# Performance work log

Hardware: AMD Instinct MI355X
Metric: run time of the kernel (lower is better)

Reference implementation:

```python
import math
import jax, jax.numpy as jnp
import numpy as np

B, T, D_IN, D_SAE, K = 256, 64, 512, 4096, 32

def _sinusoidal_posemb(T, d):
    pos = jnp.arange(T, dtype=jnp.float32)[:, None]
    div = jnp.exp(jnp.arange(0, d, 2, dtype=jnp.float32) * (-(math.log(10000.0) / d)))
    pe = jnp.zeros((T, d), dtype=jnp.float32)
    pe = pe.at[:, 0::2].set(jnp.sin(pos * div))
    pe = pe.at[:, 1::2].set(jnp.cos(pos * div))
    return pe

def setup_inputs() -> dict:
    key = jax.random.key(0)
    k0, k1, k2 = jax.random.split(key, 3)
    x = jax.random.normal(k0, (B, T, D_IN), dtype=jnp.float32)
    W_enc = jax.random.normal(k1, (D_IN, D_SAE), dtype=jnp.float32) / D_IN ** 0.5
    W_dec = jax.random.normal(k2, (D_SAE, T, D_IN), dtype=jnp.float32) / D_SAE ** 0.5
    b_enc = jnp.zeros((D_SAE,), dtype=jnp.float32)
    b_dec = jnp.zeros((T, D_IN), dtype=jnp.float32)
    return {"x": x, "W_enc": W_enc, "W_dec": W_dec, "b_enc": b_enc, "b_dec": b_dec}

def reference(x, W_enc, W_dec, b_enc, b_dec):
    pe = _sinusoidal_posemb(T, D_IN)              # (T, d_in) buffer
    x_plus = x + pe[None]                         # (B, T, d_in)
    pre = jnp.einsum('btd,ds->bs', x_plus, W_enc) + b_enc  # (B, d_sae)
    v, i = jax.lax.top_k(pre, K)                  # (B, K) each
    rows = jnp.arange(B)[:, None]
    z = jnp.zeros_like(pre).at[rows, i].set(jax.nn.relu(v))  # sparse scatter
    x_hat = jnp.einsum('bs,std->btd', z, W_dec) + b_dec      # (B, T, d_in)
    loss = jnp.mean(jnp.sum((x_hat - x) ** 2, axis=-1))
    return loss, x_hat, z
```

## Files before the change

kernel.cpp:

```cpp
#include <hip/hip_runtime.h>
#include <math.h>

#define NB 256
#define NT 64
#define DIN 512
#define DSAE 4096
#define NK 32

__global__ __launch_bounds__(512) void k_xs(const float* __restrict__ x,
                                            float* __restrict__ xs,
                                            float* __restrict__ out) {
    const int b = blockIdx.x, d = threadIdx.x;
    if (b == 0 && d == 0) out[0] = 0.f;
    int j = d >> 1;
    float freq = expf((float)(2 * j) * (-9.210340371976184f / 512.0f));
    float pes = 0.f;
    if (d & 1) {
        for (int t = 0; t < NT; ++t) pes += cosf((float)t * freq);
    } else {
        for (int t = 0; t < NT; ++t) pes += sinf((float)t * freq);
    }
    const float* xp = x + (size_t)b * NT * DIN + d;
    float acc = 0.f;
#pragma unroll 16
    for (int t = 0; t < NT; ++t) acc += xp[(size_t)t * DIN];
    xs[(size_t)b * DIN + d] = acc + pes;
}

__global__ __launch_bounds__(256) void k_pre(const float* __restrict__ xs,
                                             const float* __restrict__ W,
                                             const float* __restrict__ b_enc,
                                             float* __restrict__ pre) {
    __shared__ float xs_t[DIN][16];
    const int tid = threadIdx.x;
    const int s = blockIdx.x * 256 + tid;
    const int b0 = blockIdx.y * 16;
    for (int i = tid; i < 16 * DIN; i += 256) {
        int bb = i >> 9, d = i & 511;
        xs_t[d][bb] = xs[(size_t)(b0 + bb) * DIN + d];
    }
    __syncthreads();
    float a[16], c[16];
#pragma unroll
    for (int i = 0; i < 16; ++i) { a[i] = 0.f; c[i] = 0.f; }
    const float* wp = W + s;
#pragma unroll 2
    for (int d = 0; d < DIN; d += 2) {
        float w0 = wp[(size_t)d * DSAE];
        float w1 = wp[(size_t)(d + 1) * DSAE];
        const float4* r0 = (const float4*)&xs_t[d][0];
        const float4* r1 = (const float4*)&xs_t[d + 1][0];
#pragma unroll
        for (int q = 0; q < 4; ++q) {
            float4 u = r0[q];
            a[q*4+0] += u.x * w0; a[q*4+1] += u.y * w0;
            a[q*4+2] += u.z * w0; a[q*4+3] += u.w * w0;
            float4 t2 = r1[q];
            c[q*4+0] += t2.x * w1; c[q*4+1] += t2.y * w1;
            c[q*4+2] += t2.z * w1; c[q*4+3] += t2.w * w1;
        }
    }
    float be = b_enc[s];
#pragma unroll
    for (int bb = 0; bb < 16; ++bb)
        pre[(size_t)(b0 + bb) * DSAE + s] = a[bb] + c[bb] + be;
}

__global__ __launch_bounds__(64) void k_topk(const float* __restrict__ pre,
                                             float* __restrict__ z_out,
                                             int* __restrict__ idx_s,
                                             float* __restrict__ zv_s) {
    const int b = blockIdx.x, lane = threadIdx.x;
    const float* pr = pre + (size_t)b * DSAE;
    float* zr = z_out + (size_t)b * DSAE;
    __shared__ float lv[64 * 65];
    __shared__ float lgv[64 * 8];
    __shared__ int   lga[64 * 8];
    for (int j = lane; j < DSAE; j += 64) zr[j] = 0.f;
    const int base = lane * 65;
    float v[64];
#pragma unroll
    for (int j = 0; j < 64; ++j) v[j] = pr[j * 64 + lane];
#pragma unroll
    for (int j = 0; j < 64; ++j) lv[base + j] = v[j];
    float lmax = -INFINITY; int larg = 0;
#pragma unroll
    for (int g = 0; g < 8; ++g) {
        float m = v[g * 8]; int a = g * 8;
#pragma unroll
        for (int t = 1; t < 8; ++t)
            if (v[g * 8 + t] > m) { m = v[g * 8 + t]; a = g * 8 + t; }
        lgv[lane * 8 + g] = m; lga[lane * 8 + g] = a;
        if (m > lmax) { lmax = m; larg = a; }
    }
    __syncthreads();
    int myi = 0; float myv = 0.f;
    for (int k = 0; k < NK; ++k) {
        float bv = lmax; int be = larg * 64 + lane;
#pragma unroll
        for (int off = 32; off >= 1; off >>= 1) {
            float ov = __shfl_down(bv, off);
            int oe = __shfl_down(be, off);
            if (ov > bv || (ov == bv && oe < be)) { bv = ov; be = oe; }
        }
        bv = __shfl(bv, 0); be = __shfl(be, 0);
        if (lane == k) { myi = be; myv = bv > 0.f ? bv : 0.f; }
        if (lane == (be & 63)) {
            int j0 = be >> 6;
            lv[base + j0] = -INFINITY;
            int g0 = j0 >> 3;
            float m = -INFINITY; int a2 = g0 << 3;
            for (int t = 0; t < 8; ++t) {
                float x2 = lv[base + (g0 << 3) + t];
                if (x2 > m) { m = x2; a2 = (g0 << 3) + t; }
            }
            lgv[lane * 8 + g0] = m; lga[lane * 8 + g0] = a2;
            lmax = -INFINITY; larg = 0;
            for (int g = 0; g < 8; ++g) {
                float x2 = lgv[lane * 8 + g];
                if (x2 > lmax) { lmax = x2; larg = lga[lane * 8 + g]; }
            }
        }
    }
    int rank = 0;
#pragma unroll
    for (int j = 0; j < NK; ++j) {
        int oi = __shfl(myi, j);
        if (lane < NK && oi < myi) rank++;
    }
    if (lane < NK) {
        idx_s[b * NK + rank] = myi;
        zv_s[b * NK + rank] = myv;
        zr[myi] = myv;
    }
}

__global__ __launch_bounds__(256) void k_dec(const float* __restrict__ x,
                                             const float* __restrict__ Wd,
                                             const float* __restrict__ bd,
                                             const int* __restrict__ idx_s,
                                             const float* __restrict__ zv_s,
                                             float* __restrict__ out) {
    const int b = blockIdx.y, chunk = blockIdx.x, tid = threadIdx.x;
    __shared__ int si[NK];
    __shared__ float sz[NK];
    if (tid < NK) { si[tid] = idx_s[b * NK + tid]; sz[tid] = zv_s[b * NK + tid]; }
    __syncthreads();
    const int f0 = chunk * 1024 + tid;
    const float4* bd4 = (const float4*)bd;
    float4 acc0 = bd4[f0];
    float4 acc1 = bd4[f0 + 256];
    float4 acc2 = bd4[f0 + 512];
    float4 acc3 = bd4[f0 + 768];
    for (int k = 0; k < NK; ++k) {
        const float4* w4 = (const float4*)(Wd + (size_t)si[k] * (NT * DIN));
        float zk = sz[k];
        float4 w0 = w4[f0], w1 = w4[f0 + 256], w2 = w4[f0 + 512], w3 = w4[f0 + 768];
        acc0.x += zk * w0.x; acc0.y += zk * w0.y; acc0.z += zk * w0.z; acc0.w += zk * w0.w;
        acc1.x += zk * w1.x; acc1.y += zk * w1.y; acc1.z += zk * w1.z; acc1.w += zk * w1.w;
        acc2.x += zk * w2.x; acc2.y += zk * w2.y; acc2.z += zk * w2.z; acc2.w += zk * w2.w;
        acc3.x += zk * w3.x; acc3.y += zk * w3.y; acc3.z += zk * w3.z; acc3.w += zk * w3.w;
    }
    const float* xr = x + (size_t)b * (NT * DIN);
    float lsum = 0.f, dx;
    float xv[16];
#pragma unroll
    for (int q = 0; q < 4; ++q) {
        int e = (f0 + q * 256) * 4;
#pragma unroll
        for (int c2 = 0; c2 < 4; ++c2) xv[q * 4 + c2] = __builtin_nontemporal_load(&xr[e + c2]);
    }
    dx = acc0.x - xv[0];  lsum += dx * dx;  dx = acc0.y - xv[1];  lsum += dx * dx;
    dx = acc0.z - xv[2];  lsum += dx * dx;  dx = acc0.w - xv[3];  lsum += dx * dx;
    dx = acc1.x - xv[4];  lsum += dx * dx;  dx = acc1.y - xv[5];  lsum += dx * dx;
    dx = acc1.z - xv[6];  lsum += dx * dx;  dx = acc1.w - xv[7];  lsum += dx * dx;
    dx = acc2.x - xv[8];  lsum += dx * dx;  dx = acc2.y - xv[9];  lsum += dx * dx;
    dx = acc2.z - xv[10]; lsum += dx * dx;  dx = acc2.w - xv[11]; lsum += dx * dx;
    dx = acc3.x - xv[12]; lsum += dx * dx;  dx = acc3.y - xv[13]; lsum += dx * dx;
    dx = acc3.z - xv[14]; lsum += dx * dx;  dx = acc3.w - xv[15]; lsum += dx * dx;

    float* xh = out + 1 + (size_t)b * (NT * DIN);
    int e;
    e = f0 * 4;
    __builtin_nontemporal_store(acc0.x, &xh[e]);     __builtin_nontemporal_store(acc0.y, &xh[e+1]);
    __builtin_nontemporal_store(acc0.z, &xh[e+2]);   __builtin_nontemporal_store(acc0.w, &xh[e+3]);
    e = (f0 + 256) * 4;
    __builtin_nontemporal_store(acc1.x, &xh[e]);     __builtin_nontemporal_store(acc1.y, &xh[e+1]);
    __builtin_nontemporal_store(acc1.z, &xh[e+2]);   __builtin_nontemporal_store(acc1.w, &xh[e+3]);
    e = (f0 + 512) * 4;
    __builtin_nontemporal_store(acc2.x, &xh[e]);     __builtin_nontemporal_store(acc2.y, &xh[e+1]);
    __builtin_nontemporal_store(acc2.z, &xh[e+2]);   __builtin_nontemporal_store(acc2.w, &xh[e+3]);
    e = (f0 + 768) * 4;
    __builtin_nontemporal_store(acc3.x, &xh[e]);     __builtin_nontemporal_store(acc3.y, &xh[e+1]);
    __builtin_nontemporal_store(acc3.z, &xh[e+2]);   __builtin_nontemporal_store(acc3.w, &xh[e+3]);

#pragma unroll
    for (int off = 32; off >= 1; off >>= 1) lsum += __shfl_down(lsum, off);
    __shared__ float red[4];
    if ((tid & 63) == 0) red[tid >> 6] = lsum;
    __syncthreads();
    if (tid == 0) {
        float tot = red[0] + red[1] + red[2] + red[3];
        atomicAdd(out, tot * (1.0f / (NB * NT)));
    }
}

extern "C" void kernel_launch(void* const* d_in, const int* in_sizes, int n_in,
                              void* d_out, int out_size, void* d_ws, size_t ws_size,
                              hipStream_t stream) {
    const float* x     = (const float*)d_in[0];
    const float* W_enc = (const float*)d_in[1];
    const float* W_dec = (const float*)d_in[2];
    const float* b_enc = (const float*)d_in[3];
    const float* b_dec = (const float*)d_in[4];
    float* out = (float*)d_out;

    float* ws    = (float*)d_ws;
    float* xs    = ws;
    float* pre   = ws + 131072;
    int*   idx_s = (int*)(ws + 1179648);
    float* zv_s  = ws + 1187840;

    float* z_out = out + 1 + (size_t)NB * NT * DIN;

    k_xs<<<NB, 512, 0, stream>>>(x, xs, out);
    k_pre<<<dim3(16, 16), 256, 0, stream>>>(xs, W_enc, b_enc, pre);
    k_topk<<<NB, 64, 0, stream>>>(pre, z_out, idx_s, zv_s);
    k_dec<<<dim3(8, NB), 256, 0, stream>>>(x, W_dec, b_dec, idx_s, zv_s, out);
}
```

Baseline: 156.2 us.

## Restructure decoder to stream W_dec column slabs through shared memory once

The decoder now assigns each block a 32-element column slice, with one batch row per thread. All 4096 W_dec rows for that slice are streamed through double-buffered shared memory in windows of 64. Each thread walks its own sorted top-k indices and accumulates only the rows it needs. This reads W_dec once in total rather than gathering 32 rows per batch element, cutting global traffic. The cost is reading the whole 128 MB W_dec, 64 barrier phases per block, divergent per-thread loops, and uncoalesced x loads and output stores with per-thread row strides.

Result: slower. 361.0 us (+131.0%).

```diff
diff --git a/kernel.cpp b/kernel.cpp
--- a/kernel.cpp
+++ b/kernel.cpp
@@ -6,6 +6,9 @@
 #define DIN 512
 #define DSAE 4096
 #define NK 32
+
+typedef float f32x4 __attribute__((ext_vector_type(4)));
+typedef float f32x2 __attribute__((ext_vector_type(2)));
 
 __global__ __launch_bounds__(512) void k_xs(const float* __restrict__ x,
                                             float* __restrict__ xs,
@@ -135,64 +138,97 @@
     }
 }
 
+#define WSTRIDE 36
 __global__ __launch_bounds__(256) void k_dec(const float* __restrict__ x,
                                              const float* __restrict__ Wd,
                                              const float* __restrict__ bd,
                                              const int* __restrict__ idx_s,
                                              const float* __restrict__ zv_s,
                                              float* __restrict__ out) {
-    const int b = blockIdx.y, chunk = blockIdx.x, tid = threadIdx.x;
-    __shared__ int si[NK];
-    __shared__ float sz[NK];
-    if (tid < NK) { si[tid] = idx_s[b * NK + tid]; sz[tid] = zv_s[b * NK + tid]; }
-    __syncthreads();
-    const int f0 = chunk * 1024 + tid;
-    const float4* bd4 = (const float4*)bd;
-    float4 acc0 = bd4[f0];
-    float4 acc1 = bd4[f0 + 256];
-    float4 acc2 = bd4[f0 + 512];
-    float4 acc3 = bd4[f0 + 768];
-    for (int k = 0; k < NK; ++k) {
-        const float4* w4 = (const float4*)(Wd + (size_t)si[k] * (NT * DIN));
-        float zk = sz[k];
-        float4 w0 = w4[f0], w1 = w4[f0 + 256], w2 = w4[f0 + 512], w3 = w4[f0 + 768];
-        acc0.x += zk * w0.x; acc0.y += zk * w0.y; acc0.z += zk * w0.z; acc0.w += zk * w0.w;
-        acc1.x += zk * w1.x; acc1.y += zk * w1.y; acc1.z += zk * w1.z; acc1.w += zk * w1.w;
-        acc2.x += zk * w2.x; acc2.y += zk * w2.y; acc2.z += zk * w2.z; acc2.w += zk * w2.w;
-        acc3.x += zk * w3.x; acc3.y += zk * w3.y; acc3.z += zk * w3.z; acc3.w += zk * w3.w;
-    }
-    const float* xr = x + (size_t)b * (NT * DIN);
-    float lsum = 0.f, dx;
-    float xv[16];
-#pragma unroll
-    for (int q = 0; q < 4; ++q) {
-        int e = (f0 + q * 256) * 4;
-#pragma unroll
-        for (int c2 = 0; c2 < 4; ++c2) xv[q * 4 + c2] = __builtin_nontemporal_load(&xr[e + c2]);
-    }
-    dx = acc0.x - xv[0];  lsum += dx * dx;  dx = acc0.y - xv[1];  lsum += dx * dx;
-    dx = acc0.z - xv[2];  lsum += dx * dx;  dx = acc0.w - xv[3];  lsum += dx * dx;
-    dx = acc1.x - xv[4];  lsum += dx * dx;  dx = acc1.y - xv[5];  lsum += dx * dx;
-    dx = acc1.z - xv[6];  lsum += dx * dx;  dx = acc1.w - xv[7];  lsum += dx * dx;
-    dx = acc2.x - xv[8];  lsum += dx * dx;  dx = acc2.y - xv[9];  lsum += dx * dx;
-    dx = acc2.z - xv[10]; lsum += dx * dx;  dx = acc2.w - xv[11]; lsum += dx * dx;
-    dx = acc3.x - xv[12]; lsum += dx * dx;  dx = acc3.y - xv[13]; lsum += dx * dx;
-    dx = acc3.z - xv[14]; lsum += dx * dx;  dx = acc3.w - xv[15]; lsum += dx * dx;
-
-    float* xh = out + 1 + (size_t)b * (NT * DIN);
-    int e;
-    e = f0 * 4;
-    __builtin_nontemporal_store(acc0.x, &xh[e]);     __builtin_nontemporal_store(acc0.y, &xh[e+1]);
-    __builtin_nontemporal_store(acc0.z, &xh[e+2]);   __builtin_nontemporal_store(acc0.w, &xh[e+3]);
-    e = (f0 + 256) * 4;
-    __builtin_nontemporal_store(acc1.x, &xh[e]);     __builtin_nontemporal_store(acc1.y, &xh[e+1]);
-    __builtin_nontemporal_store(acc1.z, &xh[e+2]);   __builtin_nontemporal_store(acc1.w, &xh[e+3]);
-    e = (f0 + 512) * 4;
-    __builtin_nontemporal_store(acc2.x, &xh[e]);     __builtin_nontemporal_store(acc2.y, &xh[e+1]);
-    __builtin_nontemporal_store(acc2.z, &xh[e+2]);   __builtin_nontemporal_store(acc2.w, &xh[e+3]);
-    e = (f0 + 768) * 4;
-    __builtin_nontemporal_store(acc3.x, &xh[e]);     __builtin_nontemporal_store(acc3.y, &xh[e+1]);
-    __builtin_nontemporal_store(acc3.z, &xh[e+2]);   __builtin_nontemporal_store(acc3.w, &xh[e+3]);
+    const int tid = threadIdx.x;
+    const int cbase = blockIdx.x * 32;
+    __shared__ float buf[2][64 * WSTRIDE];
+
+    float acc[32];
+    {
+        const float4* bd4 = (const float4*)(bd + cbase);
+#pragma unroll
+        for (int q = 0; q < 8; ++q) {
+            float4 v = bd4[q];
+            acc[q*4+0] = v.x; acc[q*4+1] = v.y; acc[q*4+2] = v.z; acc[q*4+3] = v.w;
+        }
+    }
+
+    const int slot_w = tid >> 2;
+    const int quad0 = (tid & 3) * 2;
+    const float* gsrc = Wd + (size_t)slot_w * (NT * DIN) + cbase + quad0 * 4;
+
+    const int* myi = idx_s + tid * NK;
+    const float* myz = zv_s + tid * NK;
+    int p = 0;
+    int nexti = myi[0];
+    float nextz = myz[0];
+
+    float4 st0 = *(const float4*)(gsrc);
+    float4 st1 = *(const float4*)(gsrc + 4);
+    {
+        float* wb = &buf[0][slot_w * WSTRIDE + quad0 * 4];
+        *(float4*)wb = st0;
+        *(float4*)(wb + 4) = st1;
+    }
+    __syncthreads();
+
+    for (int phase = 0; phase < 64; ++phase) {
+        if (phase < 63) {
+            const float* g = gsrc + (size_t)(phase + 1) * 64 * (NT * DIN);
+            st0 = *(const float4*)(g);
+            st1 = *(const float4*)(g + 4);
+        }
+        const int win0 = phase * 64;
+        const int winEnd = win0 + 64;
+        const float* cb = buf[phase & 1];
+        while (nexti < winEnd) {
+            const float zk = nextz;
+            const float* w = cb + (nexti - win0) * WSTRIDE;
+#pragma unroll
+            for (int q = 0; q < 8; ++q) {
+                float4 wv = *(const float4*)&w[q * 4];
+                acc[q*4+0] += zk * wv.x; acc[q*4+1] += zk * wv.y;
+                acc[q*4+2] += zk * wv.z; acc[q*4+3] += zk * wv.w;
+            }
+            ++p;
+            if (p < NK) { nexti = myi[p]; nextz = myz[p]; }
+            else nexti = 0x7fffffff;
+        }
+        if (phase < 63) {
+            float* wb = &buf[(phase + 1) & 1][slot_w * WSTRIDE + quad0 * 4];
+            *(float4*)wb = st0;
+            *(float4*)(wb + 4) = st1;
+        }
+        __syncthreads();
+    }
+
+    const float* xr = x + (size_t)tid * (NT * DIN) + cbase;
+    float lsum = 0.f;
+#pragma unroll
+    for (int e = 0; e < 32; ++e) {
+        float xv = __builtin_nontemporal_load(&xr[e]);
+        float d = acc[e] - xv;
+        lsum += d * d;
+    }
+    float* xh = out + 1 + (size_t)tid * (NT * DIN) + cbase;
+    __builtin_nontemporal_store(acc[0], &xh[0]);
+    {
+        f32x2 v2; v2.x = acc[1]; v2.y = acc[2];
+        __builtin_nontemporal_store(v2, (f32x2*)(xh + 1));
+    }
+#pragma unroll
+    for (int q = 0; q < 7; ++q) {
+        f32x4 v4;
+        v4.x = acc[3+4*q]; v4.y = acc[4+4*q]; v4.z = acc[5+4*q]; v4.w = acc[6+4*q];
+        __builtin_nontemporal_store(v4, (f32x4*)(xh + 3 + 4 * q));
+    }
+    __builtin_nontemporal_store(acc[31], &xh[31]);
 
 #pragma unroll
     for (int off = 32; off >= 1; off >>= 1) lsum += __shfl_down(lsum, off);
@@ -226,5 +262,5 @@
     k_xs<<<NB, 512, 0, stream>>>(x, xs, out);
     k_pre<<<dim3(16, 16), 256, 0, stream>>>(xs, W_enc, b_enc, pre);
     k_topk<<<NB, 64, 0, stream>>>(pre, z_out, idx_s, zv_s);
-    k_dec<<<dim3(8, NB), 256, 0, stream>>>(x, W_dec, b_dec, idx_s, zv_s, out);
-}
+    k_dec<<<1024, 256, 0, stream>>>(x, W_dec, b_dec, idx_s, zv_s, out);
+}
```
